# Optimization experiments

Measured on AMD Instinct MI355X. Metric: run time of the kernel, lower is better.

Reference implementation:

```python
import jax, jax.numpy as jnp
import numpy as np

N = 100000
E = 1600000
IN_C = 64
HID = 64


def sage_conv(x, edge_index, W_l, b_l, W_r):
    # PyG SAGEConv with mean aggregation:
    # out = lin_l(mean_{j in N(i)} x_j) + lin_r(x_i)
    src, dst = edge_index[0], edge_index[1]
    msgs = x[src]                                        # [E, C] gather
    summed = jax.ops.segment_sum(msgs, dst, num_segments=N)   # [N, C]
    count = jax.ops.segment_sum(jnp.ones((edge_index.shape[1],), x.dtype), dst,
                                num_segments=N)          # [N]
    agg = summed / jnp.maximum(count, 1.0)[:, None]      # mean, safe for isolated nodes
    return agg @ W_l + b_l + x @ W_r


def setup_inputs() -> dict:
    key = jax.random.key(0)
    ks = jax.random.split(key, 10)
    x = jax.random.normal(ks[0], (N, IN_C), dtype=jnp.float32)
    edge_index = jax.random.randint(ks[1], (2, E), 0, N, dtype=jnp.int64)
    s1 = 1.0 / np.sqrt(IN_C)
    s2 = 1.0 / np.sqrt(HID)
    W_l1 = jax.random.uniform(ks[2], (IN_C, HID), jnp.float32, -s1, s1)
    b_l1 = jax.random.uniform(ks[3], (HID,), jnp.float32, -s1, s1)
    W_r1 = jax.random.uniform(ks[4], (IN_C, HID), jnp.float32, -s1, s1)
    W_l2 = jax.random.uniform(ks[5], (HID, HID), jnp.float32, -s2, s2)
    b_l2 = jax.random.uniform(ks[6], (HID,), jnp.float32, -s2, s2)
    W_r2 = jax.random.uniform(ks[7], (HID, HID), jnp.float32, -s2, s2)
    W_c = jax.random.uniform(ks[8], (HID, 1), jnp.float32, -s2, s2)
    b_c = jax.random.uniform(ks[9], (1,), jnp.float32, -s2, s2)
    return {"x": x, "edge_index": edge_index,
            "W_l1": W_l1, "b_l1": b_l1, "W_r1": W_r1,
            "W_l2": W_l2, "b_l2": b_l2, "W_r2": W_r2,
            "W_c": W_c, "b_c": b_c}


def reference(x, edge_index, W_l1, b_l1, W_r1, W_l2, b_l2, W_r2, W_c, b_c):
    h = jax.nn.relu(sage_conv(x, edge_index, W_l1, b_l1, W_r1))
    # dropout p=0.2 is identity in eval mode
    h = jax.nn.relu(sage_conv(h, edge_index, W_l2, b_l2, W_r2))
    out = (h @ W_c + b_c).squeeze(-1)   # [N]
    return out
```

## Files before the change

kernel.cpp:

```cpp
#include <hip/hip_runtime.h>


#define C 64
#define NB 196
#define BCAP 16000

typedef _Float16 half8 __attribute__((ext_vector_type(8)));
typedef float f32x4 __attribute__((ext_vector_type(4)));

static inline size_t align256(size_t x) { return (x + 255) & ~(size_t)255; }

__device__ void bucket1_part(const int* __restrict__ ei, int* __restrict__ bucketCnt,
                             unsigned* __restrict__ records, int E, int bid) {
    __shared__ int cnt[NB], cur[NB], gbase[NB];
    const int t = (int)threadIdx.x;
    for (int b = t; b < NB; b += 256) { cnt[b] = 0; cur[b] = 0; }
    __syncthreads();
    const int nE4 = E >> 2;
    const int base4 = bid * 1024;
    int4 dreg[4];
    #pragma unroll
    for (int j = 0; j < 4; ++j) {
        int i4 = base4 + j * 256 + t;
        if (i4 < nE4) {
            int4 d = ((const int4*)(ei + E))[i4];
            dreg[j] = d;
            atomicAdd(&cnt[d.x >> 9], 1);
            atomicAdd(&cnt[d.y >> 9], 1);
            atomicAdd(&cnt[d.z >> 9], 1);
            atomicAdd(&cnt[d.w >> 9], 1);
        }
    }
    __syncthreads();
    for (int b = t; b < NB; b += 256)
        gbase[b] = cnt[b] ? atomicAdd(&bucketCnt[b], cnt[b]) : 0;
    __syncthreads();
    #pragma unroll
    for (int j = 0; j < 4; ++j) {
        int i4 = base4 + j * 256 + t;
        if (i4 < nE4) {
            int4 s = ((const int4*)ei)[i4];
            int4 d = dreg[j];
            int b0 = d.x >> 9, b1 = d.y >> 9, b2 = d.z >> 9, b3 = d.w >> 9;
            int k0 = gbase[b0] + atomicAdd(&cur[b0], 1);
            int k1 = gbase[b1] + atomicAdd(&cur[b1], 1);
            int k2 = gbase[b2] + atomicAdd(&cur[b2], 1);
            int k3 = gbase[b3] + atomicAdd(&cur[b3], 1);
            if (k0 < BCAP) records[(size_t)b0 * BCAP + k0] = ((unsigned)s.x << 9) | (unsigned)(d.x & 511);
            if (k1 < BCAP) records[(size_t)b1 * BCAP + k1] = ((unsigned)s.y << 9) | (unsigned)(d.y & 511);
            if (k2 < BCAP) records[(size_t)b2 * BCAP + k2] = ((unsigned)s.z << 9) | (unsigned)(d.z & 511);
            if (k3 < BCAP) records[(size_t)b3 * BCAP + k3] = ((unsigned)s.w << 9) | (unsigned)(d.w & 511);
        }
    }
}

__device__ void cvt_part(const float* __restrict__ x, _Float16* __restrict__ xh,
                         int n8, int bid) {
    int i = bid * 256 + (int)threadIdx.x;
    if (i < n8) {
        const float4* p = (const float4*)x + (size_t)i * 2;
        float4 a = p[0], b = p[1];
        half8 h;
        h[0] = (_Float16)a.x; h[1] = (_Float16)a.y; h[2] = (_Float16)a.z; h[3] = (_Float16)a.w;
        h[4] = (_Float16)b.x; h[5] = (_Float16)b.y; h[6] = (_Float16)b.z; h[7] = (_Float16)b.w;
        ((half8*)xh)[i] = h;
    }
}

__device__ void wpack_part(const float* __restrict__ W0, const float* __restrict__ W1,
                           const float* __restrict__ W2, const float* __restrict__ W3,
                           _Float16* __restrict__ wp, int bid) {
    int t = bid * 256 + (int)threadIdx.x;
    if (t >= 2048) return;
    int lane = t & 63, step = (t >> 6) & 1, tile = (t >> 7) & 3, mat = t >> 9;
    const float* W = (mat == 0) ? W0 : (mat == 1) ? W1 : (mat == 2) ? W2 : W3;
    int col = tile * 16 + (lane & 15);
    int k0  = step * 32 + ((lane >> 4) << 3);
    half8 h;
    #pragma unroll
    for (int j = 0; j < 8; ++j) h[j] = (_Float16)W[(k0 + j) * C + col];
    ((half8*)wp)[t] = h;
}

__global__ __launch_bounds__(256) void prep_kernel(
    const int* __restrict__ ei, int* __restrict__ bucketCnt,
    unsigned* __restrict__ records, int E,
    const float* __restrict__ x, _Float16* __restrict__ xh, int n8,
    const float* __restrict__ W0, const float* __restrict__ W1,
    const float* __restrict__ W2, const float* __restrict__ W3,
    _Float16* __restrict__ wp, int bgrid, int cgrid)
{
    int bid = blockIdx.x;
    if (bid < bgrid)              bucket1_part(ei, bucketCnt, records, E, bid);
    else if (bid < bgrid + cgrid) cvt_part(x, xh, n8, bid - bgrid);
    else                          wpack_part(W0, W1, W2, W3, wp, bid - bgrid - cgrid);
}

__global__ __launch_bounds__(256) void csrbuild_kernel(
    const unsigned* __restrict__ records, const int* __restrict__ bucketCnt,
    int* __restrict__ offs, int* __restrict__ csr, int n)
{
    __shared__ int histo[512], cur[512], lofs[512], wsum[4];
    __shared__ int bb_sh;
    const int b = blockIdx.x, t = (int)threadIdx.x;
    const int lane = t & 63, wid = t >> 6;
    histo[t] = 0; histo[t + 256] = 0;
    cur[t] = 0;   cur[t + 256] = 0;
    int v = (t < NB) ? min(bucketCnt[t], BCAP) : 0;
    int si = v;
    #pragma unroll
    for (int off = 1; off < 64; off <<= 1) {
        int u = __shfl_up(si, off, 64);
        if (lane >= off) si += u;
    }
    if (lane == 63) wsum[wid] = si;
    __syncthreads();
    int wpre = 0;
    for (int w = 0; w < wid; ++w) wpre += wsum[w];
    if (t == b) bb_sh = wpre + (si - v);
    if (b == 0 && t == 0)
        offs[n] = wsum[0] + wsum[1] + wsum[2] + wsum[3];
    __syncthreads();
    const int cnt = min(bucketCnt[b], BCAP);
    const int bb = bb_sh;
    const unsigned* rec = records + (size_t)b * BCAP;
    for (int j = t; j < cnt; j += 256)
        atomicAdd(&histo[rec[j] & 511], 1);
    __syncthreads();
    int h0 = histo[2 * t], h1 = histo[2 * t + 1];
    int s = h0 + h1;
    int sj = s;
    #pragma unroll
    for (int off = 1; off < 64; off <<= 1) {
        int u = __shfl_up(sj, off, 64);
        if (lane >= off) sj += u;
    }
    __syncthreads();
    if (lane == 63) wsum[wid] = sj;
    __syncthreads();
    int wpre2 = 0;
    for (int w = 0; w < wid; ++w) wpre2 += wsum[w];
    int ex = wpre2 + (sj - s);
    lofs[2 * t] = ex;
    lofs[2 * t + 1] = ex + h0;
    int node0 = b * 512 + 2 * t;
    if (node0 < n)     offs[node0]     = bb + ex;
    if (node0 + 1 < n) offs[node0 + 1] = bb + ex + h0;
    __syncthreads();
    for (int j = t; j < cnt; j += 256) {
        unsigned r = rec[j];
        int d = (int)(r & 511u);
        int rk = atomicAdd(&cur[d], 1);
        csr[bb + lofs[d] + rk] = (int)(r >> 9);
    }
}

template <bool FINAL>
__global__ __launch_bounds__(256) void sage_kernel(
    const _Float16* __restrict__ Xh, const int* __restrict__ csr,
    const int* __restrict__ offs,
    const _Float16* __restrict__ wpL, const _Float16* __restrict__ wpR,
    const float* __restrict__ bl,
    const float* __restrict__ Wc, const float* __restrict__ bc,
    void* __restrict__ outp, int n)
{
    const int lane = threadIdx.x & 63;
    const int wid  = threadIdx.x >> 6;
    const int base = blockIdx.x * 32;
    __shared__ _Float16 Aagg[32][72];
    __shared__ float Opart[2][2][16];

    const int slot = lane >> 3;
    const int sub  = lane & 7;
    const int node = base + wid * 8 + slot;
    float acc[8] = {0.f,0.f,0.f,0.f,0.f,0.f,0.f,0.f};
    int dcount = 0;
    if (node < n) {
        int start = offs[node];
        dcount = offs[node + 1] - start;
        int k = 0;
        for (; k + 8 <= dcount; k += 8) {
            int idx[8];
            #pragma unroll
            for (int jj = 0; jj < 8; ++jj) idx[jj] = csr[start + k + jj];
            half8 v[8];
            #pragma unroll
            for (int jj = 0; jj < 8; ++jj)
                v[jj] = *(const half8*)(Xh + ((size_t)idx[jj] << 6) + (sub << 3));
            #pragma unroll
            for (int jj = 0; jj < 8; ++jj)
                #pragma unroll
                for (int j = 0; j < 8; ++j) acc[j] += (float)v[jj][j];
        }
        for (; k + 4 <= dcount; k += 4) {
            int i0 = csr[start + k + 0];
            int i1 = csr[start + k + 1];
            int i2 = csr[start + k + 2];
            int i3 = csr[start + k + 3];
            half8 v0 = *(const half8*)(Xh + ((size_t)i0 << 6) + (sub << 3));
            half8 v1 = *(const half8*)(Xh + ((size_t)i1 << 6) + (sub << 3));
            half8 v2 = *(const half8*)(Xh + ((size_t)i2 << 6) + (sub << 3));
            half8 v3 = *(const half8*)(Xh + ((size_t)i3 << 6) + (sub << 3));
            #pragma unroll
            for (int j = 0; j < 8; ++j) acc[j] += (float)v0[j];
            #pragma unroll
            for (int j = 0; j < 8; ++j) acc[j] += (float)v1[j];
            #pragma unroll
            for (int j = 0; j < 8; ++j) acc[j] += (float)v2[j];
            #pragma unroll
            for (int j = 0; j < 8; ++j) acc[j] += (float)v3[j];
        }
        for (; k < dcount; ++k) {
            int i0 = csr[start + k];
            half8 v0 = *(const half8*)(Xh + ((size_t)i0 << 6) + (sub << 3));
            #pragma unroll
            for (int j = 0; j < 8; ++j) acc[j] += (float)v0[j];
        }
    }
    float inv = 1.0f / fmaxf((float)dcount, 1.0f);
    half8 hv;
    #pragma unroll
    for (int j = 0; j < 8; ++j) hv[j] = (_Float16)(acc[j] * inv);
    *(half8*)&Aagg[wid * 8 + slot][sub * 8] = hv;
    __syncthreads();

    const int Mtile = wid >> 1;
    const int pair  = wid & 1;
    const int row16 = lane & 15;
    const int kg    = lane >> 4;
    const int myrow = base + Mtile * 16 + row16;
    const int srow  = (myrow < n) ? myrow : 0;

    half8 ag0 = *(const half8*)&Aagg[Mtile * 16 + row16][kg * 8];
    half8 ag1 = *(const half8*)&Aagg[Mtile * 16 + row16][32 + kg * 8];
    const _Float16* xrow = Xh + ((size_t)srow << 6);
    half8 xi0 = *(const half8*)(xrow + kg * 8);
    half8 xi1 = *(const half8*)(xrow + 32 + kg * 8);

    float ptot[4] = {0.f, 0.f, 0.f, 0.f};
    #pragma unroll
    for (int q = 0; q < 2; ++q) {
        const int ct = pair * 2 + q;
        const half8* BL = (const half8*)(wpL + (size_t)ct * 1024);
        const half8* BR = (const half8*)(wpR + (size_t)ct * 1024);
        half8 b0 = BL[lane];
        half8 b1 = BL[64 + lane];
        half8 b2 = BR[lane];
        half8 b3 = BR[64 + lane];
        f32x4 cacc = {0.f, 0.f, 0.f, 0.f};
        cacc = __builtin_amdgcn_mfma_f32_16x16x32_f16(ag0, b0, cacc, 0, 0, 0);
        cacc = __builtin_amdgcn_mfma_f32_16x16x32_f16(ag1, b1, cacc, 0, 0, 0);
        cacc = __builtin_amdgcn_mfma_f32_16x16x32_f16(xi0, b2, cacc, 0, 0, 0);
        cacc = __builtin_amdgcn_mfma_f32_16x16x32_f16(xi1, b3, cacc, 0, 0, 0);

        const int col = ct * 16 + row16;
        const float bias = bl[col];
        if (!FINAL) {
            _Float16* h1 = (_Float16*)outp;
            #pragma unroll
            for (int j = 0; j < 4; ++j) {
                int r = base + Mtile * 16 + kg * 4 + j;
                if (r < n) {
                    float v = fmaxf(cacc[j] + bias, 0.f);
                    h1[((size_t)r << 6) + col] = (_Float16)v;
                }
            }
        } else {
            const float wc = Wc[col];
            float p[4];
            #pragma unroll
            for (int j = 0; j < 4; ++j) p[j] = fmaxf(cacc[j] + bias, 0.f) * wc;
            #pragma unroll
            for (int off = 1; off < 16; off <<= 1) {
                #pragma unroll
                for (int j = 0; j < 4; ++j) p[j] += __shfl_xor(p[j], off, 64);
            }
            #pragma unroll
            for (int j = 0; j < 4; ++j) ptot[j] += p[j];
        }
    }

    if (FINAL) {
        if (row16 == 0) {
            #pragma unroll
            for (int j = 0; j < 4; ++j) Opart[Mtile][pair][kg * 4 + j] = ptot[j];
        }
        __syncthreads();
        const int tid = threadIdx.x;
        if (tid < 32) {
            int Mt = tid >> 4, r = tid & 15;
            int gr = base + Mt * 16 + r;
            if (gr < n)
                ((float*)outp)[gr] = Opart[Mt][0][r] + Opart[Mt][1][r] + bc[0];
        }
    }
}

extern "C" void kernel_launch(void* const* d_in, const int* in_sizes, int n_in,
                              void* d_out, int out_size, void* d_ws, size_t ws_size,
                              hipStream_t stream) {
    const float* x   = (const float*)d_in[0];
    const int*   ei  = (const int*)d_in[1];
    const float* Wl1 = (const float*)d_in[2];
    const float* bl1 = (const float*)d_in[3];
    const float* Wr1 = (const float*)d_in[4];
    const float* Wl2 = (const float*)d_in[5];
    const float* bl2 = (const float*)d_in[6];
    const float* Wr2 = (const float*)d_in[7];
    const float* Wc  = (const float*)d_in[8];
    const float* bc  = (const float*)d_in[9];
    float* out = (float*)d_out;

    const int N = in_sizes[0] / C;
    const int E = in_sizes[1] / 2;

    char* ws = (char*)d_ws;
    size_t off = 0;
    int* offs      = (int*)(ws + off); off += align256((size_t)(N + 1) * 4);
    int* bucketCnt = (int*)(ws + off); off += align256((size_t)NB * 4);
    int* csr       = (int*)(ws + off); off += align256((size_t)E * 4);
    size_t h1_sz = (size_t)N * C * 2;
    size_t rec_sz = (size_t)NB * BCAP * 4;
    _Float16* h1 = (_Float16*)(ws + off); off += align256(h1_sz > rec_sz ? h1_sz : rec_sz);
    _Float16* xh = (_Float16*)(ws + off); off += align256((size_t)N * C * 2);
    _Float16* wp = (_Float16*)(ws + off); off += align256((size_t)2048 * 8 * 2);
    if (off > ws_size) return;

    unsigned* records = (unsigned*)h1;

    const int blk = 256;
    const int n8 = N * C / 8;
    const int cgrid = (n8 + blk - 1) / blk;
    const int nE4 = E >> 2;
    const int bgrid = (nE4 + 1023) / 1024;

    hipMemsetAsync(bucketCnt, 0, (size_t)NB * 4, stream);
    prep_kernel<<<bgrid + cgrid + 8, blk, 0, stream>>>(
        ei, bucketCnt, records, E, x, xh, n8, Wl1, Wr1, Wl2, Wr2, wp, bgrid, cgrid);
    csrbuild_kernel<<<NB, blk, 0, stream>>>(records, bucketCnt, offs, csr, N);

    const int node_grid = (N + 31) / 32;
    sage_kernel<false><<<node_grid, blk, 0, stream>>>(
        xh, csr, offs, wp, wp + 4096, bl1, nullptr, nullptr, h1, N);
    sage_kernel<true><<<node_grid, blk, 0, stream>>>(
        h1, csr, offs, wp + 8192, wp + 12288, bl2, Wc, bc, out, N);
}
```

Before: 204.6 us.

## Sort nodes by in-degree so each wave processes similar-degree nodes

Builds a degree histogram during CSR construction and adds a kernel that produces a permutation of node ids grouped by in-degree (capped at 63). Both SAGE kernels then read their node ids through this permutation, so the 8 nodes sharing a wave have similar neighbour counts and the gather loops diverge less. The cost is an extra kernel launch, one more indirection, and scattered row writes for h1 and the output, which lose the coalescing and locality of contiguous node ranges.

After: 209.5 us. 1.02x slower.

```diff
diff --git a/kernel.cpp b/kernel.cpp
--- a/kernel.cpp
+++ b/kernel.cpp
@@ -98,14 +98,15 @@
 
 __global__ __launch_bounds__(256) void csrbuild_kernel(
     const unsigned* __restrict__ records, const int* __restrict__ bucketCnt,
-    int* __restrict__ offs, int* __restrict__ csr, int n)
+    int* __restrict__ offs, int* __restrict__ csr, int* __restrict__ degHist, int n)
 {
-    __shared__ int histo[512], cur[512], lofs[512], wsum[4];
+    __shared__ int histo[512], cur[512], lofs[512], wsum[4], degH[64];
     __shared__ int bb_sh;
     const int b = blockIdx.x, t = (int)threadIdx.x;
     const int lane = t & 63, wid = t >> 6;
     histo[t] = 0; histo[t + 256] = 0;
     cur[t] = 0;   cur[t + 256] = 0;
+    if (t < 64) degH[t] = 0;
     int v = (t < NB) ? min(bucketCnt[t], BCAP) : 0;
     int si = v;
     #pragma unroll
@@ -144,9 +145,10 @@
     lofs[2 * t] = ex;
     lofs[2 * t + 1] = ex + h0;
     int node0 = b * 512 + 2 * t;
-    if (node0 < n)     offs[node0]     = bb + ex;
-    if (node0 + 1 < n) offs[node0 + 1] = bb + ex + h0;
-    __syncthreads();
+    if (node0 < n)     { offs[node0]     = bb + ex;      atomicAdd(&degH[min(h0, 63)], 1); }
+    if (node0 + 1 < n) { offs[node0 + 1] = bb + ex + h0; atomicAdd(&degH[min(h1, 63)], 1); }
+    __syncthreads();
+    if (t < 64 && degH[t]) atomicAdd(&degHist[t], degH[t]);
     for (int j = t; j < cnt; j += 256) {
         unsigned r = rec[j];
         int d = (int)(r & 511u);
@@ -155,10 +157,52 @@
     }
 }
 
+__global__ __launch_bounds__(256) void permbuild_kernel(
+    const int* __restrict__ offs, const int* __restrict__ degHist,
+    int* __restrict__ degCursor, int* __restrict__ perm, int n)
+{
+    __shared__ int degBase[64], cnt[64], cur[64], gb[64];
+    const int t = (int)threadIdx.x;
+    if (t < 64) {
+        int v = degHist[t];
+        int si = v;
+        #pragma unroll
+        for (int off = 1; off < 64; off <<= 1) {
+            int u = __shfl_up(si, off, 64);
+            if (t >= off) si += u;
+        }
+        degBase[t] = si - v;
+        cnt[t] = 0; cur[t] = 0;
+    }
+    __syncthreads();
+    const int base = blockIdx.x * 1024;
+    int mybin[4];
+    #pragma unroll
+    for (int j = 0; j < 4; ++j) {
+        int i = base + j * 256 + t;
+        if (i < n) {
+            int deg = offs[i + 1] - offs[i];
+            mybin[j] = min(deg, 63);
+            atomicAdd(&cnt[mybin[j]], 1);
+        } else mybin[j] = -1;
+    }
+    __syncthreads();
+    if (t < 64) gb[t] = cnt[t] ? atomicAdd(&degCursor[t], cnt[t]) : 0;
+    __syncthreads();
+    #pragma unroll
+    for (int j = 0; j < 4; ++j) {
+        int i = base + j * 256 + t;
+        if (mybin[j] >= 0) {
+            int rk = atomicAdd(&cur[mybin[j]], 1);
+            perm[degBase[mybin[j]] + gb[mybin[j]] + rk] = i;
+        }
+    }
+}
+
 template <bool FINAL>
 __global__ __launch_bounds__(256) void sage_kernel(
     const _Float16* __restrict__ Xh, const int* __restrict__ csr,
-    const int* __restrict__ offs,
+    const int* __restrict__ offs, const int* __restrict__ perm,
     const _Float16* __restrict__ wpL, const _Float16* __restrict__ wpR,
     const float* __restrict__ bl,
     const float* __restrict__ Wc, const float* __restrict__ bc,
@@ -172,21 +216,22 @@
 
     const int slot = lane >> 3;
     const int sub  = lane & 7;
-    const int node = base + wid * 8 + slot;
+    const int idx  = base + wid * 8 + slot;
     float acc[8] = {0.f,0.f,0.f,0.f,0.f,0.f,0.f,0.f};
     int dcount = 0;
-    if (node < n) {
+    if (idx < n) {
+        const int node = perm[idx];
         int start = offs[node];
         dcount = offs[node + 1] - start;
         int k = 0;
         for (; k + 8 <= dcount; k += 8) {
-            int idx[8];
-            #pragma unroll
-            for (int jj = 0; jj < 8; ++jj) idx[jj] = csr[start + k + jj];
+            int idv[8];
+            #pragma unroll
+            for (int jj = 0; jj < 8; ++jj) idv[jj] = csr[start + k + jj];
             half8 v[8];
             #pragma unroll
             for (int jj = 0; jj < 8; ++jj)
-                v[jj] = *(const half8*)(Xh + ((size_t)idx[jj] << 6) + (sub << 3));
+                v[jj] = *(const half8*)(Xh + ((size_t)idv[jj] << 6) + (sub << 3));
             #pragma unroll
             for (int jj = 0; jj < 8; ++jj)
                 #pragma unroll
@@ -228,8 +273,8 @@
     const int pair  = wid & 1;
     const int row16 = lane & 15;
     const int kg    = lane >> 4;
-    const int myrow = base + Mtile * 16 + row16;
-    const int srow  = (myrow < n) ? myrow : 0;
+    const int myidx = base + Mtile * 16 + row16;
+    const int srow  = (myidx < n) ? perm[myidx] : 0;
 
     half8 ag0 = *(const half8*)&Aagg[Mtile * 16 + row16][kg * 8];
     half8 ag1 = *(const half8*)&Aagg[Mtile * 16 + row16][32 + kg * 8];
@@ -259,10 +304,11 @@
             _Float16* h1 = (_Float16*)outp;
             #pragma unroll
             for (int j = 0; j < 4; ++j) {
-                int r = base + Mtile * 16 + kg * 4 + j;
-                if (r < n) {
-                    float v = fmaxf(cacc[j] + bias, 0.f);
-                    h1[((size_t)r << 6) + col] = (_Float16)v;
+                int ridx = base + Mtile * 16 + kg * 4 + j;
+                if (ridx < n) {
+                    int gr = perm[ridx];
+                    float vv = fmaxf(cacc[j] + bias, 0.f);
+                    h1[((size_t)gr << 6) + col] = (_Float16)vv;
                 }
             }
         } else {
@@ -289,9 +335,9 @@
         const int tid = threadIdx.x;
         if (tid < 32) {
             int Mt = tid >> 4, r = tid & 15;
-            int gr = base + Mt * 16 + r;
-            if (gr < n)
-                ((float*)outp)[gr] = Opart[Mt][0][r] + Opart[Mt][1][r] + bc[0];
+            int ridx = base + Mt * 16 + r;
+            if (ridx < n)
+                ((float*)outp)[perm[ridx]] = Opart[Mt][0][r] + Opart[Mt][1][r] + bc[0];
         }
     }
 }
@@ -317,13 +363,17 @@
     char* ws = (char*)d_ws;
     size_t off = 0;
     int* offs      = (int*)(ws + off); off += align256((size_t)(N + 1) * 4);
-    int* bucketCnt = (int*)(ws + off); off += align256((size_t)NB * 4);
+    int* bucketCnt = (int*)(ws + off);
+    int* degHist   = (int*)(ws + off + 1024);
+    int* degCursor = (int*)(ws + off + 1280);
+    off += 1536;
     int* csr       = (int*)(ws + off); off += align256((size_t)E * 4);
     size_t h1_sz = (size_t)N * C * 2;
     size_t rec_sz = (size_t)NB * BCAP * 4;
     _Float16* h1 = (_Float16*)(ws + off); off += align256(h1_sz > rec_sz ? h1_sz : rec_sz);
     _Float16* xh = (_Float16*)(ws + off); off += align256((size_t)N * C * 2);
     _Float16* wp = (_Float16*)(ws + off); off += align256((size_t)2048 * 8 * 2);
+    int* perm    = (int*)(ws + off); off += align256((size_t)N * 4);
     if (off > ws_size) return;
 
     unsigned* records = (unsigned*)h1;
@@ -333,15 +383,17 @@
     const int cgrid = (n8 + blk - 1) / blk;
     const int nE4 = E >> 2;
     const int bgrid = (nE4 + 1023) / 1024;
-
-    hipMemsetAsync(bucketCnt, 0, (size_t)NB * 4, stream);
+    const int pgrid = (N + 1023) / 1024;
+
+    hipMemsetAsync(bucketCnt, 0, 1536, stream);
     prep_kernel<<<bgrid + cgrid + 8, blk, 0, stream>>>(
         ei, bucketCnt, records, E, x, xh, n8, Wl1, Wr1, Wl2, Wr2, wp, bgrid, cgrid);
-    csrbuild_kernel<<<NB, blk, 0, stream>>>(records, bucketCnt, offs, csr, N);
+    csrbuild_kernel<<<NB, blk, 0, stream>>>(records, bucketCnt, offs, csr, degHist, N);
+    permbuild_kernel<<<pgrid, blk, 0, stream>>>(offs, degHist, degCursor, perm, N);
 
     const int node_grid = (N + 31) / 32;
     sage_kernel<false><<<node_grid, blk, 0, stream>>>(
-        xh, csr, offs, wp, wp + 4096, bl1, nullptr, nullptr, h1, N);
+        xh, csr, offs, perm, wp, wp + 4096, bl1, nullptr, nullptr, h1, N);
     sage_kernel<true><<<node_grid, blk, 0, stream>>>(
-        h1, csr, offs, wp + 8192, wp + 12288, bl2, Wc, bc, out, N);
-}
+        h1, csr, offs, perm, wp + 8192, wp + 12288, bl2, Wc, bc, out, N);
+}
```
